# Kernel tuning notes

Measured on AMD Instinct MI355X. Metric: run time of the kernel, lower is better.

Reference implementation:

```python
import math
import jax, jax.numpy as jnp
import numpy as np

B, L, D, H = 2, 2048, 1024, 16
DK = D // H
N_TYPES = 6  # token types; < 3 => prompt (U/O/E), >= 3 => item (I)


def setup_inputs() -> dict:
    key = jax.random.key(0)
    ks = jax.random.split(key, 8)
    w_scale = 0.02
    return {
        "x": jax.random.normal(ks[0], (B, L, D), dtype=jnp.float32),
        "token_types": jax.random.randint(ks[1], (B, L), 0, N_TYPES, dtype=jnp.int32),
        "seq_lens": jax.random.randint(ks[2], (B,), L // 2, L + 1, dtype=jnp.int32),
        "W_q": jax.random.normal(ks[3], (D, D), dtype=jnp.float32) * w_scale,
        "W_k": jax.random.normal(ks[4], (D, D), dtype=jnp.float32) * w_scale,
        "W_v": jax.random.normal(ks[5], (D, D), dtype=jnp.float32) * w_scale,
        "W_u": jax.random.normal(ks[6], (D, D), dtype=jnp.float32) * w_scale,
        "W_o": jax.random.normal(ks[7], (D, D), dtype=jnp.float32) * w_scale,
    }


def reference(x, token_types, seq_lens, W_q, W_k, W_v, W_u, W_o):
    b, l, d = x.shape
    neg = jnp.finfo(x.dtype).min

    def proj(W):  # torch Linear (no bias): y = x @ W.T -> (b, H, l, dk)
        return jnp.einsum("bld,ed->ble", x, W).reshape(b, l, H, DK).transpose(0, 2, 1, 3)

    Q, K, V, U = proj(W_q), proj(W_k), proj(W_v), proj(W_u)

    scores = jnp.einsum("bhid,bhjd->bhij", Q, K) / math.sqrt(DK)  # (b,H,l,l)

    # Hybrid mask: causal (-inf above diagonal), but 0 wherever key j is a
    # prompt token (prompt<->prompt bidirectional, item->prompt allowed).
    is_prompt = token_types < 3                      # (b, l)
    causal = jnp.where(jnp.triu(jnp.ones((l, l), dtype=bool), k=1), neg, 0.0).astype(x.dtype)
    mask = jnp.where(is_prompt[:, None, :], jnp.asarray(0.0, x.dtype), causal[None, :, :])  # (b,l,l)
    scores = scores + mask[:, None, :, :]

    # Padding mask on key positions j >= seq_len
    pad = jnp.arange(l)[None, :] >= seq_lens[:, None]  # (b, l)
    scores = jnp.where(pad[:, None, None, :], neg, scores)

    attn = jax.nn.softmax(scores, axis=-1)
    out = jnp.einsum("bhij,bhjd->bhid", attn, V) * U   # HSTU pointwise gating
    out = out.transpose(0, 2, 1, 3).reshape(b, l, d)
    return jnp.einsum("bld,ed->ble", out, W_o)
```

## Files before the change

kernel.cpp:

```cpp
#include <hip/hip_runtime.h>


#define L_SEQ 2048

typedef __attribute__((ext_vector_type(8))) short bf16x8;
typedef __attribute__((ext_vector_type(8))) unsigned short u16x8;
typedef __attribute__((ext_vector_type(4))) float f32x4;
typedef __attribute__((ext_vector_type(16))) float f32x16;

#if __has_builtin(__builtin_amdgcn_exp2f)
#define EXP2F __builtin_amdgcn_exp2f
#else
#define EXP2F __builtin_exp2f
#endif

__device__ __forceinline__ unsigned short f2bf(float f) {
  union { float f; unsigned u; } c; c.f = f;
  unsigned r = c.u + 0x7FFFu + ((c.u >> 16) & 1u);
  return (unsigned short)(r >> 16);
}
__device__ __forceinline__ float bf2f(unsigned short h) {
  union { unsigned u; float f; } c; c.u = ((unsigned)h) << 16;
  return c.f;
}

__device__ __forceinline__ void async16(const void* g, void* l) {
  __builtin_amdgcn_global_load_lds((__attribute__((address_space(1))) void*)g,
                                   (__attribute__((address_space(3))) void*)l,
                                   16, 0, 0);
}

__device__ __forceinline__ unsigned cvtpk_bf16(float lo, float hi) {
  unsigned r; asm("v_cvt_pk_bf16_f32 %0, %1, %2" : "=v"(r) : "v"(lo), "v"(hi));
  return r;
}

__global__ __launch_bounds__(256) void cvt_all(
    const float* __restrict__ x,
    const float* __restrict__ wq, const float* __restrict__ wk,
    const float* __restrict__ wv, const float* __restrict__ wu,
    const float* __restrict__ wo,
    unsigned short* __restrict__ xb, unsigned short* __restrict__ wcat) {
  const int seg = blockIdx.x >> 10;
  const float* s;
  unsigned short* d;
  float sc = 1.0f;
  if (seg < 4)      { s = x + (size_t)seg * 1048576;  d = xb + (size_t)seg * 1048576; }
  else {
    const int ws = seg - 4;
    s = ws == 0 ? wq : ws == 1 ? wk : ws == 2 ? wv : ws == 3 ? wu : wo;
    d = wcat + (size_t)ws * 1048576;
    if (ws == 0) sc = 0.18033688011112042f;
  }
  const int i = ((blockIdx.x & 1023) * 256 + threadIdx.x) * 4;
  const float4 v = *reinterpret_cast<const float4*>(s + i);
  ushort4 o;
  o.x = f2bf(v.x * sc); o.y = f2bf(v.y * sc); o.z = f2bf(v.z * sc); o.w = f2bf(v.w * sc);
  *reinterpret_cast<ushort4*>(d + i) = o;
}

__global__ __launch_bounds__(256) void vtrans(const unsigned short* __restrict__ qkvu,
                                              unsigned short* __restrict__ vtg,
                                              const int* __restrict__ tt,
                                              const int* __restrict__ sl,
                                              unsigned* __restrict__ allowed) {
  __shared__ unsigned short tileb[4096];
  const int t = blockIdx.x, h = blockIdx.y, b = blockIdx.z;
  const size_t rb = (size_t)b * L_SEQ * 4096;
  const int tid = threadIdx.x;
  const int vp = tid & 31, vd0 = (tid >> 5) * 8;
  const int j0 = t * 64;
  if (h == 0 && tid < 64) {
    const int j = j0 + tid;
    const unsigned long long m = __ballot((tt[b * L_SEQ + j] < 3) && (j < sl[b]));
    if (tid == 0) {
      allowed[b * 64 + 2 * t]     = (unsigned)m;
      allowed[b * 64 + 2 * t + 1] = (unsigned)(m >> 32);
    }
  }
  const u16x8 g0 = *reinterpret_cast<const u16x8*>(
      qkvu + rb + (size_t)(j0 + 2 * vp) * 4096 + 2048 + h * 64 + vd0);
  const u16x8 g1 = *reinterpret_cast<const u16x8*>(
      qkvu + rb + (size_t)(j0 + 2 * vp + 1) * 4096 + 2048 + h * 64 + vd0);
  #pragma unroll
  for (int e = 0; e < 8; ++e) {
    const int d = vd0 + e;
    const unsigned pk = (unsigned)g0[e] | ((unsigned)g1[e] << 16);
    *reinterpret_cast<unsigned*>((char*)tileb +
        d * 128 + 16 * ((vp >> 2) ^ (d & 7)) + 4 * (vp & 3)) = pk;
  }
  __syncthreads();
  const size_t ob = ((size_t)(b * 16 + h) * 32 + t) * 4096;
  *reinterpret_cast<u16x8*>(vtg + ob + tid * 16) =
      *reinterpret_cast<const u16x8*>(tileb + tid * 16);
  *reinterpret_cast<u16x8*>(vtg + ob + tid * 16 + 8) =
      *reinterpret_cast<const u16x8*>(tileb + tid * 16 + 8);
}

__global__ __launch_bounds__(512, 2) void gemm256_bt(
    const unsigned short* __restrict__ A,
    const unsigned short* __restrict__ BT,
    unsigned short* __restrict__ Cb, int K, int N)
{
  __shared__ char smem[131072];

  const int tid = threadIdx.x, w = tid >> 6, lane = tid & 63;
  const int lo = lane & 15, hi = lane >> 4;
  const int wm = w >> 2, wn = w & 3;
  const int d = blockIdx.x;
  const int lin = (d & 7) * 32 + (d >> 3);
  const int i0 = (lin >> 4) * 256, j0 = (lin & 15) * 256;

  const int rr = lane >> 3, ch = lane & 7;
  const int ksw = 8 * (ch ^ rr);

  auto stage = [&](int buf, int t) {
    const size_t k0 = (size_t)t * 64 + ksw;
    #pragma unroll
    for (int q = 0; q < 2; ++q) {
      const int p = 2 * w + q;
      const int row = 8 * p + rr;
      #pragma unroll
      for (int h = 0; h < 2; ++h) {
        async16(A  + (size_t)(i0 + h * 128 + row) * K + k0,
                smem + buf * 32768 + h * 16384 + p * 1024);
        async16(BT + (size_t)(j0 + h * 128 + row) * K + k0,
                smem + 65536 + buf * 32768 + h * 16384 + p * 1024);
      }
    }
  };

  f32x4 acc[8][4] = {};
  stage(0, 0);

  const int nt = K >> 6;
  for (int u = 0; u < nt; ++u) {
    const int buf = u & 1;
    if (u + 1 < nt) {
      stage(buf ^ 1, u + 1);
      asm volatile("s_waitcnt vmcnt(8)" ::: "memory");
    } else {
      asm volatile("s_waitcnt vmcnt(0)" ::: "memory");
    }
    __builtin_amdgcn_s_barrier();
    __builtin_amdgcn_sched_barrier(0);

    const char* Ah = smem + buf * 32768 + wm * 16384;
    const char* Bh = smem + 65536 + buf * 32768 + (wn >> 1) * 16384;
    const int brow0 = (wn & 1) * 64;

    bf16x8 bfr[4][2];
    #pragma unroll
    for (int n = 0; n < 4; ++n)
      #pragma unroll
      for (int ks = 0; ks < 2; ++ks)
        bfr[n][ks] = *reinterpret_cast<const bf16x8*>(
            Bh + (brow0 + n * 16 + lo) * 128 + 16 * ((ks * 4 + hi) ^ (lo & 7)));

    #pragma unroll
    for (int ph = 0; ph < 4; ++ph) {
      bf16x8 afr[2][2];
      #pragma unroll
      for (int mm = 0; mm < 2; ++mm)
        #pragma unroll
        for (int ks = 0; ks < 2; ++ks)
          afr[mm][ks] = *reinterpret_cast<const bf16x8*>(
              Ah + ((ph * 2 + mm) * 16 + lo) * 128 + 16 * ((ks * 4 + hi) ^ (lo & 7)));
      __builtin_amdgcn_s_barrier();
      __builtin_amdgcn_sched_barrier(0);
      __builtin_amdgcn_s_setprio(1);
      #pragma unroll
      for (int ks = 0; ks < 2; ++ks)
        #pragma unroll
        for (int mm = 0; mm < 2; ++mm)
          #pragma unroll
          for (int n = 0; n < 4; ++n)
            acc[ph * 2 + mm][n] = __builtin_amdgcn_mfma_f32_16x16x32_bf16(
                afr[mm][ks], bfr[n][ks], acc[ph * 2 + mm][n], 0, 0, 0);
      __builtin_amdgcn_s_setprio(0);
      __builtin_amdgcn_s_barrier();
      __builtin_amdgcn_sched_barrier(0);
    }
  }

  #pragma unroll
  for (int m = 0; m < 8; ++m) {
    const int row = i0 + wm * 128 + m * 16 + hi * 4;
    #pragma unroll
    for (int n = 0; n < 4; ++n) {
      const int col = j0 + wn * 64 + n * 16 + lo;
      #pragma unroll
      for (int r = 0; r < 4; ++r)
        Cb[(size_t)(row + r) * N + col] = f2bf(acc[m][n][r]);
    }
  }
}

template<int OUT_BF16>
__global__ __launch_bounds__(256) void gemm_bt(
    const unsigned short* __restrict__ A,
    const unsigned short* __restrict__ BT,
    float* __restrict__ Cf, unsigned short* __restrict__ Cb,
    int M, int N, int K, int cpx, int nbxm, int nbxs)
{
  __shared__ unsigned short As[2][128 * 32];
  __shared__ unsigned short Bs[2][128 * 32];

  const int tid = threadIdx.x;
  const int w = tid >> 6, lane = tid & 63;
  const int lo = lane & 15, hi = lane >> 4;
  const int d = blockIdx.x + gridDim.x * blockIdx.y;
  const int lin = (d & 7) * cpx + (d >> 3);
  const int i0 = (lin >> nbxs) * 128, j0 = (lin & nbxm) * 128;
  const int wr = w >> 1, wc = w & 1;
  const int c0 = w * 2, rsub = lane >> 2, csub = (lane & 3) * 8;

  f32x4 acc[4][4] = {};

  #pragma unroll
  for (int q = 0; q < 2; ++q) {
    const int c = c0 + q;
    async16(A  + (size_t)(i0 + c * 16 + rsub) * K + csub, &As[0][c * 512]);
    async16(BT + (size_t)(j0 + c * 16 + rsub) * K + csub, &Bs[0][c * 512]);
  }
  __syncthreads();

  const int nt = K >> 5;
  for (int t = 0; t < nt; ++t) {
    const int buf = t & 1;
    if (t + 1 < nt) {
      const int k0 = (t + 1) << 5;
      #pragma unroll
      for (int q = 0; q < 2; ++q) {
        const int c = c0 + q;
        async16(A  + (size_t)(i0 + c * 16 + rsub) * K + k0 + csub, &As[buf ^ 1][c * 512]);
        async16(BT + (size_t)(j0 + c * 16 + rsub) * K + k0 + csub, &Bs[buf ^ 1][c * 512]);
      }
    }
    bf16x8 a[4], b[4];
    #pragma unroll
    for (int m = 0; m < 4; ++m)
      a[m] = *reinterpret_cast<const bf16x8*>(&As[buf][(wr * 64 + m * 16 + lo) * 32 + hi * 8]);
    #pragma unroll
    for (int n = 0; n < 4; ++n)
      b[n] = *reinterpret_cast<const bf16x8*>(&Bs[buf][(wc * 64 + n * 16 + lo) * 32 + hi * 8]);
    #pragma unroll
    for (int m = 0; m < 4; ++m)
      #pragma unroll
      for (int n = 0; n < 4; ++n)
        acc[m][n] = __builtin_amdgcn_mfma_f32_16x16x32_bf16(a[m], b[n], acc[m][n], 0, 0, 0);
    __syncthreads();
  }

  #pragma unroll
  for (int m = 0; m < 4; ++m) {
    const int row = i0 + wr * 64 + m * 16 + hi * 4;
    #pragma unroll
    for (int n = 0; n < 4; ++n) {
      const int col = j0 + wc * 64 + n * 16 + lo;
      #pragma unroll
      for (int r = 0; r < 4; ++r) {
        if (OUT_BF16) Cb[(size_t)(row + r) * N + col] = f2bf(acc[m][n][r]);
        else          Cf[(size_t)(row + r) * N + col] = acc[m][n][r];
      }
    }
  }
}

__global__ __launch_bounds__(512, 4) void hstu_attn(
    const unsigned short* __restrict__ qkvu,
    const unsigned short* __restrict__ vtg,
    const unsigned* __restrict__ allowed,
    const int* __restrict__ slens,
    unsigned short* __restrict__ gated)
{
  __shared__ char smem[65536];

  const int dlin = blockIdx.x + (blockIdx.y << 4) + (blockIdx.z << 8);
  const int lin = ((dlin & 7) << 6) | (dlin >> 3);
  const int qt = lin & 15, h = (lin >> 4) & 15, b = lin >> 8;
  const int i0 = qt * 128;
  const int tid = threadIdx.x, w = tid >> 6, lane = tid & 63;
  const int g = w >> 2, wq = w & 3;
  const int c = lane & 31, sb = lane >> 5;
  const int seqlen = slens[b];
  const size_t rb = (size_t)b * L_SEQ * 4096;
  const size_t vb = (size_t)(b * 16 + h) * 32 * 4096;
  const int qrow = i0 + wq * 32 + c;

  auto stageK = [&](int buf, int t) {
    const int j0 = t * 64;
    char* Kb = smem + (g * 2 + buf) * 8192;
    #pragma unroll
    for (int q = 0; q < 2; ++q) {
      const int p = wq * 2 + q;
      const int krow = 8 * p + (lane >> 3);
      const int d0 = 8 * ((lane & 7) ^ (lane >> 3));
      async16(qkvu + rb + (size_t)(j0 + krow) * 4096 + 1024 + h * 64 + d0,
              Kb + p * 1024);
    }
  };
  auto stageV = [&](int buf, int t) {
    char* Vb = smem + 32768 + (g * 2 + buf) * 8192;
    #pragma unroll
    for (int q = 0; q < 2; ++q) {
      const int p = wq * 2 + q;
      async16(vtg + vb + (size_t)t * 4096 + p * 512 + lane * 8, Vb + p * 1024);
    }
  };

  const int nt = (seqlen + 63) >> 6;
  const int niter = (nt + 1) >> 1;

  stageK(0, g); stageV(0, g);

  bf16x8 qf[4];
  #pragma unroll
  for (int kd = 0; kd < 4; ++kd)
    qf[kd] = *reinterpret_cast<const bf16x8*>(
        qkvu + rb + (size_t)qrow * 4096 + h * 64 + kd * 16 + sb * 8);
  const unsigned pmword = allowed[b * 64 + lane];
  const int limb = (qrow < seqlen - 1 ? qrow : seqlen - 1) - 4 * sb;

  f32x16 o0 = {}, o1 = {};
  float rs = 0.f;

  asm volatile("s_waitcnt vmcnt(0)" ::: "memory");
  __builtin_amdgcn_s_barrier();
  __builtin_amdgcn_sched_barrier(0);

  for (int i = 0; i < niter; ++i) {
    const int t = 2 * i + g;
    const bool active = t < nt;
    const int buf = i & 1;
    const int j0 = t * 64;
    const bool pre = (t + 2 < nt);

    if (active) {
      if (pre) { stageK(buf ^ 1, t + 2); stageV(buf ^ 1, t + 2); }

      const char* Kb = smem + (g * 2 + buf) * 8192;
      const char* Vb = smem + 32768 + (g * 2 + buf) * 8192;
      const bool fast = (j0 + 64 <= seqlen) && (j0 + 63 <= i0 + wq * 32);

      #pragma unroll
      for (int z = 0; z < 2; ++z) {
        f32x16 s = {};
        __builtin_amdgcn_s_setprio(1);
        #pragma unroll
        for (int kd = 0; kd < 4; ++kd) {
          const bf16x8 kf = *reinterpret_cast<const bf16x8*>(
              Kb + (32 * z + c) * 128 + (((2 * kd + sb) ^ (c & 7)) << 4));
          s = __builtin_amdgcn_mfma_f32_32x32x16_bf16(kf, qf[kd], s, 0, 0, 0);
        }
        __builtin_amdgcn_s_setprio(0);

        if (fast) {
          #pragma unroll
          for (int r = 0; r < 16; ++r) { s[r] = EXP2F(s[r]); rs += s[r]; }
        } else {
          const unsigned pmz = __builtin_amdgcn_readlane(pmword, 2 * t + z);
          const int lim = limb - j0 - 32 * z;
          const unsigned cm = lim < 0 ? 0u : (lim >= 31 ? ~0u : ((2u << lim) - 1u));
          const unsigned al = (pmz >> (4 * sb)) | cm;
          #pragma unroll
          for (int r = 0; r < 16; ++r) {
            const int kc = (r & 3) + 8 * (r >> 2);
            const float p = EXP2F(s[r]);
            s[r] = ((al >> kc) & 1) ? p : 0.f;
            rs += s[r];
          }
        }

        unsigned U0, U1, W0, W1;
        U0 = cvtpk_bf16(s[0], s[1]);  U1 = cvtpk_bf16(s[2], s[3]);
        W0 = cvtpk_bf16(s[4], s[5]);  W1 = cvtpk_bf16(s[6], s[7]);
        asm("v_permlane32_swap_b32 %0, %1" : "+v"(U0), "+v"(W0));
        asm("v_permlane32_swap_b32 %0, %1" : "+v"(U1), "+v"(W1));
        union { unsigned u[4]; bf16x8 v; } pu;
        pu.u[0] = U0; pu.u[1] = U1; pu.u[2] = W0; pu.u[3] = W1;
        const bf16x8 pfE = pu.v;
        U0 = cvtpk_bf16(s[8], s[9]);   U1 = cvtpk_bf16(s[10], s[11]);
        W0 = cvtpk_bf16(s[12], s[13]); W1 = cvtpk_bf16(s[14], s[15]);
        asm("v_permlane32_swap_b32 %0, %1" : "+v"(U0), "+v"(W0));
        asm("v_permlane32_swap_b32 %0, %1" : "+v"(U1), "+v"(W1));
        pu.u[0] = U0; pu.u[1] = U1; pu.u[2] = W0; pu.u[3] = W1;
        const bf16x8 pfO = pu.v;

        const int kpE = 2 * z, kpO = 2 * z + 1;
        const int swE = ((2 * kpE + sb) ^ (c & 7)) << 4;
        const int swO = ((2 * kpO + sb) ^ (c & 7)) << 4;
        const bf16x8 ve0 = *reinterpret_cast<const bf16x8*>(Vb + c * 128 + swE);
        const bf16x8 ve1 = *reinterpret_cast<const bf16x8*>(Vb + (32 + c) * 128 + swE);
        const bf16x8 vo0 = *reinterpret_cast<const bf16x8*>(Vb + c * 128 + swO);
        const bf16x8 vo1 = *reinterpret_cast<const bf16x8*>(Vb + (32 + c) * 128 + swO);
        __builtin_amdgcn_s_setprio(1);
        o0 = __builtin_amdgcn_mfma_f32_32x32x16_bf16(ve0, pfE, o0, 0, 0, 0);
        o1 = __builtin_amdgcn_mfma_f32_32x32x16_bf16(ve1, pfE, o1, 0, 0, 0);
        o0 = __builtin_amdgcn_mfma_f32_32x32x16_bf16(vo0, pfO, o0, 0, 0, 0);
        o1 = __builtin_amdgcn_mfma_f32_32x32x16_bf16(vo1, pfO, o1, 0, 0, 0);
        __builtin_amdgcn_s_setprio(0);
      }
      asm volatile("s_waitcnt vmcnt(0)" ::: "memory");
    }
    __builtin_amdgcn_s_barrier();
    __builtin_amdgcn_sched_barrier(0);
  }

  const float lsum = rs + __shfl_xor(rs, 32, 64);

  float* cb = (float*)smem;
  const int col = wq * 64 + lane;
  if (g == 1) {
    #pragma unroll
    for (int r = 0; r < 16; ++r) {
      cb[r * 260 + col]        = o0[r];
      cb[(16 + r) * 260 + col] = o1[r];
    }
    cb[32 * 260 + col] = lsum;
  }
  __syncthreads();
  if (g == 1) return;
  #pragma unroll
  for (int r = 0; r < 16; ++r) {
    o0[r] += cb[r * 260 + col];
    o1[r] += cb[(16 + r) * 260 + col];
  }
  const float rin = 1.0f / (lsum + cb[32 * 260 + col]);

  #pragma unroll
  for (int n = 0; n < 2; ++n) {
    const f32x16 o = n ? o1 : o0;
    #pragma unroll
    for (int rq = 0; rq < 4; ++rq) {
      const int d0 = n * 32 + 8 * rq + 4 * sb;
      const ushort4 uu = *reinterpret_cast<const ushort4*>(
          qkvu + rb + (size_t)qrow * 4096 + 3072 + h * 64 + d0);
      ushort4 gg;
      gg.x = f2bf(o[4 * rq + 0] * rin * bf2f(uu.x));
      gg.y = f2bf(o[4 * rq + 1] * rin * bf2f(uu.y));
      gg.z = f2bf(o[4 * rq + 2] * rin * bf2f(uu.z));
      gg.w = f2bf(o[4 * rq + 3] * rin * bf2f(uu.w));
      *reinterpret_cast<ushort4*>(
          gated + (size_t)(b * L_SEQ + qrow) * 1024 + h * 64 + d0) = gg;
    }
  }
}

extern "C" void kernel_launch(void* const* d_in, const int* in_sizes, int n_in,
                              void* d_out, int out_size, void* d_ws, size_t ws_size,
                              hipStream_t stream) {
  const float* x  = (const float*)d_in[0];
  const int* tt   = (const int*)d_in[1];
  const int* sl   = (const int*)d_in[2];
  const float* Wq = (const float*)d_in[3];
  const float* Wk = (const float*)d_in[4];
  const float* Wv = (const float*)d_in[5];
  const float* Wu = (const float*)d_in[6];
  const float* Wo = (const float*)d_in[7];
  float* out = (float*)d_out;

  unsigned* allowed     = (unsigned*)d_ws;
  unsigned short* xb    = (unsigned short*)d_ws + 256;
  unsigned short* wcat  = xb    + (size_t)4096 * 1024;
  unsigned short* wob   = wcat  + (size_t)4096 * 1024;
  unsigned short* qkvu  = wob   + (size_t)1024 * 1024;
  unsigned short* gated = qkvu  + (size_t)4096 * 4096;
  unsigned short* vtg   = xb;

  cvt_all<<<9216, 256, 0, stream>>>(x, Wq, Wk, Wv, Wu, Wo, xb, wcat);

  gemm256_bt<<<256, 512, 0, stream>>>(xb, wcat, qkvu, 1024, 4096);

  vtrans<<<dim3(32, 16, 2), 256, 0, stream>>>(qkvu, vtg, tt, sl, allowed);

  hstu_attn<<<dim3(16, 16, 2), 512, 0, stream>>>(qkvu, vtg, allowed, sl, gated);

  gemm_bt<0><<<dim3(8, 32), 256, 0, stream>>>(gated, wob, out, nullptr,
                                              4096, 1024, 1024, 32, 7, 3);
}
```

Baseline: 127.9 us.

## Fuse V transpose into QKVU GEMM epilogue and split outputs per matrix

The QKVU projection GEMM now writes Q, K and U into separate contiguous [B*L,1024] planes. For the V columns it transposes each tile through LDS and writes the swizzled V image directly, which removes the separate vtrans kernel and its extra global round trip. Mask building moves to a tiny standalone kernel. The attention row sum is now computed with an extra MFMA against a ones vector instead of scalar adds plus a shuffle. The output GEMM switches to 64-row tiles so it launches twice as many blocks, at the cost of less reuse per block.

```diff
diff --git a/kernel.cpp b/kernel.cpp
--- a/kernel.cpp
+++ b/kernel.cpp
@@ -59,48 +59,23 @@
   *reinterpret_cast<ushort4*>(d + i) = o;
 }
 
-__global__ __launch_bounds__(256) void vtrans(const unsigned short* __restrict__ qkvu,
-                                              unsigned short* __restrict__ vtg,
-                                              const int* __restrict__ tt,
-                                              const int* __restrict__ sl,
-                                              unsigned* __restrict__ allowed) {
-  __shared__ unsigned short tileb[4096];
-  const int t = blockIdx.x, h = blockIdx.y, b = blockIdx.z;
-  const size_t rb = (size_t)b * L_SEQ * 4096;
-  const int tid = threadIdx.x;
-  const int vp = tid & 31, vd0 = (tid >> 5) * 8;
-  const int j0 = t * 64;
-  if (h == 0 && tid < 64) {
-    const int j = j0 + tid;
-    const unsigned long long m = __ballot((tt[b * L_SEQ + j] < 3) && (j < sl[b]));
-    if (tid == 0) {
-      allowed[b * 64 + 2 * t]     = (unsigned)m;
-      allowed[b * 64 + 2 * t + 1] = (unsigned)(m >> 32);
-    }
-  }
-  const u16x8 g0 = *reinterpret_cast<const u16x8*>(
-      qkvu + rb + (size_t)(j0 + 2 * vp) * 4096 + 2048 + h * 64 + vd0);
-  const u16x8 g1 = *reinterpret_cast<const u16x8*>(
-      qkvu + rb + (size_t)(j0 + 2 * vp + 1) * 4096 + 2048 + h * 64 + vd0);
-  #pragma unroll
-  for (int e = 0; e < 8; ++e) {
-    const int d = vd0 + e;
-    const unsigned pk = (unsigned)g0[e] | ((unsigned)g1[e] << 16);
-    *reinterpret_cast<unsigned*>((char*)tileb +
-        d * 128 + 16 * ((vp >> 2) ^ (d & 7)) + 4 * (vp & 3)) = pk;
-  }
-  __syncthreads();
-  const size_t ob = ((size_t)(b * 16 + h) * 32 + t) * 4096;
-  *reinterpret_cast<u16x8*>(vtg + ob + tid * 16) =
-      *reinterpret_cast<const u16x8*>(tileb + tid * 16);
-  *reinterpret_cast<u16x8*>(vtg + ob + tid * 16 + 8) =
-      *reinterpret_cast<const u16x8*>(tileb + tid * 16 + 8);
+__global__ __launch_bounds__(64) void maskbuild(const int* __restrict__ tt,
+                                                const int* __restrict__ sl,
+                                                unsigned* __restrict__ allowed) {
+  const int b = blockIdx.x >> 5, wv = blockIdx.x & 31;
+  const int j = wv * 64 + threadIdx.x;
+  const int seqlen = sl[b];
+  const unsigned long long m = __ballot((tt[b * L_SEQ + j] < 3) && (j < seqlen));
+  if (threadIdx.x == 0) {
+    allowed[b * 64 + 2 * wv]     = (unsigned)m;
+    allowed[b * 64 + 2 * wv + 1] = (unsigned)(m >> 32);
+  }
 }
 
 __global__ __launch_bounds__(512, 2) void gemm256_bt(
     const unsigned short* __restrict__ A,
     const unsigned short* __restrict__ BT,
-    unsigned short* __restrict__ Cb, int K, int N)
+    unsigned short* __restrict__ Cb, int K)
 {
   __shared__ char smem[131072];
 
@@ -183,27 +158,61 @@
     }
   }
 
-  #pragma unroll
-  for (int m = 0; m < 8; ++m) {
-    const int row = i0 + wm * 128 + m * 16 + hi * 4;
-    #pragma unroll
-    for (int n = 0; n < 4; ++n) {
-      const int col = j0 + wn * 64 + n * 16 + lo;
-      #pragma unroll
-      for (int r = 0; r < 4; ++r)
-        Cb[(size_t)(row + r) * N + col] = f2bf(acc[m][n][r]);
-    }
-  }
-}
-
-template<int OUT_BF16>
+  const int mi = (lin & 15) >> 2;
+  const int cb0 = j0 & 1023;
+  if (mi != 2) {
+    unsigned short* base = Cb + (size_t)mi * 4194304;
+    #pragma unroll
+    for (int m = 0; m < 8; ++m) {
+      const int row = i0 + wm * 128 + m * 16 + hi * 4;
+      #pragma unroll
+      for (int n = 0; n < 4; ++n) {
+        const int col = cb0 + wn * 64 + n * 16 + lo;
+        #pragma unroll
+        for (int r = 0; r < 4; ++r)
+          base[(size_t)(row + r) * 1024 + col] = f2bf(acc[m][n][r]);
+      }
+    }
+  } else {
+    #pragma unroll
+    for (int m = 0; m < 8; ++m) {
+      const int tl = (wm << 1) + (m >> 2);
+      #pragma unroll
+      for (int n = 0; n < 4; ++n) {
+        const int dd = n * 16 + lo;
+        char* ib = smem + (tl * 4 + wn) * 8192 + dd * 128;
+        const int swd = dd & 7;
+        #pragma unroll
+        for (int r = 0; r < 4; ++r) {
+          const int k = (m * 16 + hi * 4 + r) & 63;
+          *(unsigned short*)(ib + 16 * ((k >> 3) ^ swd) + 2 * (k & 7)) =
+              f2bf(acc[m][n][r]);
+        }
+      }
+    }
+    __builtin_amdgcn_s_barrier();
+    unsigned short* V = Cb + (size_t)2 * 4194304;
+    const int bI = i0 >> 11;
+    const int t0 = (i0 & 2047) >> 6;
+    const int h0 = cb0 >> 6;
+    #pragma unroll
+    for (int img = 0; img < 16; ++img) {
+      const int tl = img >> 2, hl = img & 3;
+      const size_t ob = ((size_t)(bI * 16 + h0 + hl) * 32 + (t0 + tl)) * 4096;
+      *reinterpret_cast<u16x8*>(V + ob + tid * 8) =
+          *reinterpret_cast<const u16x8*>(smem + img * 8192 + tid * 16);
+    }
+  }
+}
+
+template<int OUT_BF16, int MF>
 __global__ __launch_bounds__(256) void gemm_bt(
     const unsigned short* __restrict__ A,
     const unsigned short* __restrict__ BT,
     float* __restrict__ Cf, unsigned short* __restrict__ Cb,
     int M, int N, int K, int cpx, int nbxm, int nbxs)
 {
-  __shared__ unsigned short As[2][128 * 32];
+  __shared__ unsigned short As[2][MF * 32 * 32];
   __shared__ unsigned short Bs[2][128 * 32];
 
   const int tid = threadIdx.x;
@@ -211,41 +220,41 @@
   const int lo = lane & 15, hi = lane >> 4;
   const int d = blockIdx.x + gridDim.x * blockIdx.y;
   const int lin = (d & 7) * cpx + (d >> 3);
-  const int i0 = (lin >> nbxs) * 128, j0 = (lin & nbxm) * 128;
+  const int i0 = (lin >> nbxs) * (MF * 32), j0 = (lin & nbxm) * 128;
   const int wr = w >> 1, wc = w & 1;
-  const int c0 = w * 2, rsub = lane >> 2, csub = (lane & 3) * 8;
-
-  f32x4 acc[4][4] = {};
-
-  #pragma unroll
-  for (int q = 0; q < 2; ++q) {
-    const int c = c0 + q;
-    async16(A  + (size_t)(i0 + c * 16 + rsub) * K + csub, &As[0][c * 512]);
-    async16(BT + (size_t)(j0 + c * 16 + rsub) * K + csub, &Bs[0][c * 512]);
-  }
+  const int rsub = lane >> 2, csub = (lane & 3) * 8;
+
+  f32x4 acc[MF][4] = {};
+
+  auto stage = [&](int buf, int k0) {
+    #pragma unroll
+    for (int q = 0; q < 2; ++q) {
+      const int cB = w * 2 + q;
+      async16(BT + (size_t)(j0 + cB * 16 + rsub) * K + k0 + csub, &Bs[buf][cB * 512]);
+      if (q < MF / 2) {
+        const int cA = w * (MF / 2) + q;
+        async16(A + (size_t)(i0 + cA * 16 + rsub) * K + k0 + csub, &As[buf][cA * 512]);
+      }
+    }
+  };
+
+  stage(0, 0);
   __syncthreads();
 
   const int nt = K >> 5;
   for (int t = 0; t < nt; ++t) {
     const int buf = t & 1;
-    if (t + 1 < nt) {
-      const int k0 = (t + 1) << 5;
-      #pragma unroll
-      for (int q = 0; q < 2; ++q) {
-        const int c = c0 + q;
-        async16(A  + (size_t)(i0 + c * 16 + rsub) * K + k0 + csub, &As[buf ^ 1][c * 512]);
-        async16(BT + (size_t)(j0 + c * 16 + rsub) * K + k0 + csub, &Bs[buf ^ 1][c * 512]);
-      }
-    }
-    bf16x8 a[4], b[4];
-    #pragma unroll
-    for (int m = 0; m < 4; ++m)
-      a[m] = *reinterpret_cast<const bf16x8*>(&As[buf][(wr * 64 + m * 16 + lo) * 32 + hi * 8]);
+    if (t + 1 < nt) stage(buf ^ 1, (t + 1) << 5);
+    bf16x8 a[MF], b[4];
+    #pragma unroll
+    for (int m = 0; m < MF; ++m)
+      a[m] = *reinterpret_cast<const bf16x8*>(
+          &As[buf][(wr * (MF * 16) + m * 16 + lo) * 32 + hi * 8]);
     #pragma unroll
     for (int n = 0; n < 4; ++n)
       b[n] = *reinterpret_cast<const bf16x8*>(&Bs[buf][(wc * 64 + n * 16 + lo) * 32 + hi * 8]);
     #pragma unroll
-    for (int m = 0; m < 4; ++m)
+    for (int m = 0; m < MF; ++m)
       #pragma unroll
       for (int n = 0; n < 4; ++n)
         acc[m][n] = __builtin_amdgcn_mfma_f32_16x16x32_bf16(a[m], b[n], acc[m][n], 0, 0, 0);
@@ -253,8 +262,8 @@
   }
 
   #pragma unroll
-  for (int m = 0; m < 4; ++m) {
-    const int row = i0 + wr * 64 + m * 16 + hi * 4;
+  for (int m = 0; m < MF; ++m) {
+    const int row = i0 + wr * (MF * 16) + m * 16 + hi * 4;
     #pragma unroll
     for (int n = 0; n < 4; ++n) {
       const int col = j0 + wc * 64 + n * 16 + lo;
@@ -268,8 +277,10 @@
 }
 
 __global__ __launch_bounds__(512, 4) void hstu_attn(
-    const unsigned short* __restrict__ qkvu,
-    const unsigned short* __restrict__ vtg,
+    const unsigned short* __restrict__ qm,
+    const unsigned short* __restrict__ km,
+    const unsigned short* __restrict__ vimg,
+    const unsigned short* __restrict__ um,
     const unsigned* __restrict__ allowed,
     const int* __restrict__ slens,
     unsigned short* __restrict__ gated)
@@ -284,7 +295,7 @@
   const int g = w >> 2, wq = w & 3;
   const int c = lane & 31, sb = lane >> 5;
   const int seqlen = slens[b];
-  const size_t rb = (size_t)b * L_SEQ * 4096;
+  const size_t rbm = (size_t)b * L_SEQ * 1024;
   const size_t vb = (size_t)(b * 16 + h) * 32 * 4096;
   const int qrow = i0 + wq * 32 + c;
 
@@ -296,8 +307,7 @@
       const int p = wq * 2 + q;
       const int krow = 8 * p + (lane >> 3);
       const int d0 = 8 * ((lane & 7) ^ (lane >> 3));
-      async16(qkvu + rb + (size_t)(j0 + krow) * 4096 + 1024 + h * 64 + d0,
-              Kb + p * 1024);
+      async16(km + rbm + (size_t)(j0 + krow) * 1024 + h * 64 + d0, Kb + p * 1024);
     }
   };
   auto stageV = [&](int buf, int t) {
@@ -305,7 +315,7 @@
     #pragma unroll
     for (int q = 0; q < 2; ++q) {
       const int p = wq * 2 + q;
-      async16(vtg + vb + (size_t)t * 4096 + p * 512 + lane * 8, Vb + p * 1024);
+      async16(vimg + vb + (size_t)t * 4096 + p * 512 + lane * 8, Vb + p * 1024);
     }
   };
 
@@ -318,12 +328,15 @@
   #pragma unroll
   for (int kd = 0; kd < 4; ++kd)
     qf[kd] = *reinterpret_cast<const bf16x8*>(
-        qkvu + rb + (size_t)qrow * 4096 + h * 64 + kd * 16 + sb * 8);
+        qm + rbm + (size_t)qrow * 1024 + h * 64 + kd * 16 + sb * 8);
   const unsigned pmword = allowed[b * 64 + lane];
   const int limb = (qrow < seqlen - 1 ? qrow : seqlen - 1) - 4 * sb;
 
-  f32x16 o0 = {}, o1 = {};
-  float rs = 0.f;
+  union { unsigned u[4]; bf16x8 v; } one_;
+  one_.u[0] = one_.u[1] = one_.u[2] = one_.u[3] = 0x3F803F80u;
+  const bf16x8 onesv = one_.v;
+
+  f32x16 o0 = {}, o1 = {}, ls = {};
 
   asm volatile("s_waitcnt vmcnt(0)" ::: "memory");
   __builtin_amdgcn_s_barrier();
@@ -357,7 +370,7 @@
 
         if (fast) {
           #pragma unroll
-          for (int r = 0; r < 16; ++r) { s[r] = EXP2F(s[r]); rs += s[r]; }
+          for (int r = 0; r < 16; ++r) s[r] = EXP2F(s[r]);
         } else {
           const unsigned pmz = __builtin_amdgcn_readlane(pmword, 2 * t + z);
           const int lim = limb - j0 - 32 * z;
@@ -368,7 +381,6 @@
             const int kc = (r & 3) + 8 * (r >> 2);
             const float p = EXP2F(s[r]);
             s[r] = ((al >> kc) & 1) ? p : 0.f;
-            rs += s[r];
           }
         }
 
@@ -397,8 +409,10 @@
         __builtin_amdgcn_s_setprio(1);
         o0 = __builtin_amdgcn_mfma_f32_32x32x16_bf16(ve0, pfE, o0, 0, 0, 0);
         o1 = __builtin_amdgcn_mfma_f32_32x32x16_bf16(ve1, pfE, o1, 0, 0, 0);
+        ls = __builtin_amdgcn_mfma_f32_32x32x16_bf16(onesv, pfE, ls, 0, 0, 0);
         o0 = __builtin_amdgcn_mfma_f32_32x32x16_bf16(vo0, pfO, o0, 0, 0, 0);
         o1 = __builtin_amdgcn_mfma_f32_32x32x16_bf16(vo1, pfO, o1, 0, 0, 0);
+        ls = __builtin_amdgcn_mfma_f32_32x32x16_bf16(onesv, pfO, ls, 0, 0, 0);
         __builtin_amdgcn_s_setprio(0);
       }
       asm volatile("s_waitcnt vmcnt(0)" ::: "memory");
@@ -407,7 +421,7 @@
     __builtin_amdgcn_sched_barrier(0);
   }
 
-  const float lsum = rs + __shfl_xor(rs, 32, 64);
+  const float lsum = ls[0];
 
   float* cb = (float*)smem;
   const int col = wq * 64 + lane;
@@ -435,7 +449,7 @@
     for (int rq = 0; rq < 4; ++rq) {
       const int d0 = n * 32 + 8 * rq + 4 * sb;
       const ushort4 uu = *reinterpret_cast<const ushort4*>(
-          qkvu + rb + (size_t)qrow * 4096 + 3072 + h * 64 + d0);
+          um + rbm + (size_t)qrow * 1024 + h * 64 + d0);
       ushort4 gg;
       gg.x = f2bf(o[4 * rq + 0] * rin * bf2f(uu.x));
       gg.y = f2bf(o[4 * rq + 1] * rin * bf2f(uu.y));
@@ -466,16 +480,17 @@
   unsigned short* wob   = wcat  + (size_t)4096 * 1024;
   unsigned short* qkvu  = wob   + (size_t)1024 * 1024;
   unsigned short* gated = qkvu  + (size_t)4096 * 4096;
-  unsigned short* vtg   = xb;
 
   cvt_all<<<9216, 256, 0, stream>>>(x, Wq, Wk, Wv, Wu, Wo, xb, wcat);
 
-  gemm256_bt<<<256, 512, 0, stream>>>(xb, wcat, qkvu, 1024, 4096);
-
-  vtrans<<<dim3(32, 16, 2), 256, 0, stream>>>(qkvu, vtg, tt, sl, allowed);
-
-  hstu_attn<<<dim3(16, 16, 2), 512, 0, stream>>>(qkvu, vtg, allowed, sl, gated);
-
-  gemm_bt<0><<<dim3(8, 32), 256, 0, stream>>>(gated, wob, out, nullptr,
-                                              4096, 1024, 1024, 32, 7, 3);
-}
+  gemm256_bt<<<256, 512, 0, stream>>>(xb, wcat, qkvu, 1024);
+
+  maskbuild<<<64, 64, 0, stream>>>(tt, sl, allowed);
+
+  hstu_attn<<<dim3(16, 16, 2), 512, 0, stream>>>(
+      qkvu, qkvu + (size_t)4194304, qkvu + (size_t)2 * 4194304,
+      qkvu + (size_t)3 * 4194304, allowed, sl, gated);
+
+  gemm_bt<0, 2><<<dim3(8, 64), 256, 0, stream>>>(gated, wob, out, nullptr,
+                                                 4096, 1024, 1024, 64, 7, 3);
+}
```

Result: faster. 120.5 us (-5.8%).
